# Performance work log

Hardware: AMD Instinct MI355X
Metric: run time of the kernel (lower is better)

Reference implementation:

```python
import jax, jax.numpy as jnp
import numpy as np

B, S, D_MODEL, H, D_KV = 2, 2048, 1024, 16, 64
NUM_BUCKETS, MAX_DIST = 32, 128


def _relative_position_bucket(rel_pos, num_buckets=NUM_BUCKETS, max_distance=MAX_DIST):
    # bidirectional (encoder) bucketing, matching T5Attention._relative_position_bucket
    nb = num_buckets // 2
    buckets = (rel_pos > 0).astype(jnp.int32) * nb
    rel = jnp.abs(rel_pos)
    max_exact = nb // 2
    is_small = rel < max_exact
    rel_f = jnp.maximum(rel.astype(jnp.float32), 1.0)  # guard log(0); masked by is_small anyway
    large = max_exact + (
        jnp.log(rel_f / max_exact) / np.log(max_distance / max_exact) * (nb - max_exact)
    ).astype(jnp.int32)
    large = jnp.minimum(large, nb - 1)
    return buckets + jnp.where(is_small, rel, large)


def setup_inputs() -> dict:
    key = jax.random.key(0)
    ks = jax.random.split(key, 6)
    sc = 1.0 / np.sqrt(D_MODEL)
    return {
        "hidden_states": jax.random.normal(ks[0], (B, S, D_MODEL), jnp.float32),
        "Wq": jax.random.normal(ks[1], (D_MODEL, H * D_KV), jnp.float32) * sc,
        "Wk": jax.random.normal(ks[2], (D_MODEL, H * D_KV), jnp.float32) * sc,
        "Wv": jax.random.normal(ks[3], (D_MODEL, H * D_KV), jnp.float32) * sc,
        "Wo": jax.random.normal(ks[4], (H * D_KV, D_MODEL), jnp.float32) * sc,
        "rel_bias_table": jax.random.normal(ks[5], (NUM_BUCKETS, H), jnp.float32),
    }


def reference(hidden_states, Wq, Wk, Wv, Wo, rel_bias_table):
    b, s, _ = hidden_states.shape
    # projections (T5 uses no bias, scale=1.0 in attention)
    q = (hidden_states @ Wq).reshape(b, s, H, D_KV).transpose(0, 2, 1, 3)  # bhsd
    k = (hidden_states @ Wk).reshape(b, s, H, D_KV).transpose(0, 2, 1, 3)
    v = (hidden_states @ Wv).reshape(b, s, H, D_KV).transpose(0, 2, 1, 3)

    # relative position bias: [1, H, S, S]
    ctx = jnp.arange(s)[:, None]
    mem = jnp.arange(s)[None, :]
    buckets = _relative_position_bucket(mem - ctx)          # [S, S]
    pos_bias = rel_bias_table[buckets]                       # [S, S, H]
    pos_bias = pos_bias.transpose(2, 0, 1)[None]             # [1, H, S, S]

    scores = jnp.einsum("bhqd,bhkd->bhqk", q, k) + pos_bias  # scale = 1.0
    probs = jax.nn.softmax(scores, axis=-1)
    attn = jnp.einsum("bhqk,bhkd->bhqd", probs, v)
    attn = attn.transpose(0, 2, 1, 3).reshape(b, s, H * D_KV)
    return attn @ Wo
```

## Files before the change

kernel.cpp:

```cpp
#include <hip/hip_runtime.h>
#include <hip/hip_fp16.h>

#define S_LEN 2048
#define NH 16
#define DK 64
#define DM 1024
#define NB 2
#define QKV_SZ (NB * NH * S_LEN * DK)

typedef _Float16 half8 __attribute__((ext_vector_type(8)));
typedef _Float16 half4v __attribute__((ext_vector_type(4)));
typedef __fp16 fp16x2 __attribute__((ext_vector_type(2)));
typedef float f32x4 __attribute__((ext_vector_type(4)));

static __device__ __forceinline__ half4v pack4(const f32x4 v) {
  fp16x2 lo = __builtin_amdgcn_cvt_pkrtz(v[0], v[1]);
  fp16x2 hi = __builtin_amdgcn_cvt_pkrtz(v[2], v[3]);
  half4v r;
  ((fp16x2*)&r)[0] = lo;
  ((fp16x2*)&r)[1] = hi;
  return r;
}

#define GLL(gp, lp)                                                              \
  __builtin_amdgcn_global_load_lds(                                              \
      (const __attribute__((address_space(1))) unsigned int*)(gp),               \
      (__attribute__((address_space(3))) unsigned int*)(lp), 16, 0, 0)

__global__ __launch_bounds__(256) void prep_kernel(
    const float* __restrict__ hs, const float* __restrict__ Wq,
    const float* __restrict__ Wk, const float* __restrict__ Wv,
    const float* __restrict__ Wo, _Float16* __restrict__ Xh,
    _Float16* __restrict__ Wqkvt, _Float16* __restrict__ Wot) {
  const int z = blockIdx.z;
  const int t = threadIdx.x;
  if (z < 4) {
    __shared__ float tile[32][33];
    const float* W = (z == 0) ? Wq : (z == 1) ? Wk : (z == 2) ? Wv : Wo;
    _Float16* Wt = (z < 3) ? (Wqkvt + (size_t)z * 1048576) : Wot;
    float scale = (z == 0) ? 1.44269504f : 1.0f;
    int tx = t & 31, ty = t >> 5;
    int nx = blockIdx.x * 32 + tx;
    int ky = blockIdx.y * 32;
#pragma unroll
    for (int i = 0; i < 32; i += 8) tile[ty + i][tx] = W[(size_t)(ky + ty + i) * DM + nx];
    __syncthreads();
    int kx = ky + tx;
    int ny = blockIdx.x * 32;
#pragma unroll
    for (int i = 0; i < 32; i += 8)
      Wt[(size_t)(ny + ty + i) * DM + kx] = (_Float16)(tile[tx][ty + i] * scale);
  } else {
    const int blk = blockIdx.x + (blockIdx.y << 5);
    const int n4 = (NB * S_LEN * DM) / 4;
    for (int i = blk * 256 + t; i < n4; i += 1024 * 256) {
      float4 v = ((const float4*)hs)[i];
      half4v o;
      o[0] = (_Float16)v.x; o[1] = (_Float16)v.y; o[2] = (_Float16)v.z; o[3] = (_Float16)v.w;
      ((half4v*)Xh)[i] = o;
    }
  }
}

template <int MODE>
__global__ __launch_bounds__(256) void gemm_f16(const _Float16* __restrict__ A,
                                                const _Float16* __restrict__ Bt,
                                                void* __restrict__ Cout,
                                                int M, int N, int K) {
  __shared__ _Float16 As[2][128 * 32];
  __shared__ _Float16 Bs[2][128 * 32];
  const int t = threadIdx.x;
  const int gx = gridDim.x;
  const int nwg = gx * gridDim.y;
  const int orig = blockIdx.x + gx * blockIdx.y;
  const int wg = (orig & 7) * (nwg >> 3) + (orig >> 3);
  const int m0 = (wg / gx) * 128, n0 = (wg % gx) * 128;
  const int w = t >> 6, lane = t & 63, l15 = lane & 15, quad = lane >> 4;
  const int wr = (w >> 1) * 64, wc = (w & 1) * 64;
  const int swz = (quad ^ (l15 & 3)) * 8;

  const int row0_ = t >> 2, cg0 = (t & 3) ^ (row0_ & 3);
  const int row1_ = (t + 256) >> 2, cg1 = ((t + 256) & 3) ^ (row1_ & 3);
  const int aof0 = row0_ * K + cg0 * 8, aof1 = row1_ * K + cg1 * 8;
  const int lda = t * 16, ldb = (t + 256) * 16;

  f32x4 acc[4][4];
#pragma unroll
  for (int i = 0; i < 4; i++)
#pragma unroll
    for (int j = 0; j < 4; j++) acc[i][j] = (f32x4){0.f, 0.f, 0.f, 0.f};

#define GSTAGE(bs, kk)                                                     \
  do {                                                                     \
    const _Float16* ap_ = A + (size_t)m0 * K + (kk);                       \
    const _Float16* bp_ = Bt + (size_t)n0 * K + (kk);                      \
    GLL(ap_ + aof0, (char*)As[bs] + lda);                                  \
    GLL(ap_ + aof1, (char*)As[bs] + ldb);                                  \
    GLL(bp_ + aof0, (char*)Bs[bs] + lda);                                  \
    GLL(bp_ + aof1, (char*)Bs[bs] + ldb);                                  \
  } while (0)

  GSTAGE(0, 0);
  __syncthreads();

#define GTILE(c, kk)                                                          \
  do {                                                                        \
    if ((kk) + 32 < K) GSTAGE((c) ^ 1, (kk) + 32);                            \
    half8 af[4], bf[4];                                                       \
    _Pragma("unroll") for (int i = 0; i < 4; i++)                             \
        af[i] = *(const half8*)(As[c] + (wr + i * 16 + l15) * 32 + swz);      \
    _Pragma("unroll") for (int i = 0; i < 4; i++)                             \
        bf[i] = *(const half8*)(Bs[c] + (wc + i * 16 + l15) * 32 + swz);      \
    _Pragma("unroll") for (int i = 0; i < 4; i++)                             \
        _Pragma("unroll") for (int j = 0; j < 4; j++)                         \
            acc[i][j] =                                                       \
                __builtin_amdgcn_mfma_f32_16x16x32_f16(af[i], bf[j], acc[i][j], 0, 0, 0); \
    __syncthreads();                                                          \
  } while (0)

  for (int k0 = 0; k0 < K; k0 += 64) {
    GTILE(0, k0);
    GTILE(1, k0 + 32);
  }
#undef GTILE
#undef GSTAGE

#pragma unroll
  for (int i = 0; i < 4; i++)
#pragma unroll
    for (int j = 0; j < 4; j++) {
      int row0 = m0 + wr + i * 16 + quad * 4;
      int col = n0 + wc + j * 16 + l15;
      if (MODE == 1) {
#pragma unroll
        for (int r = 0; r < 4; r++)
          ((float*)Cout)[(size_t)(row0 + r) * N + col] = acc[i][j][r];
      } else {
        int which = col >> 10, rem = col & 1023, hh = rem >> 6, dd = rem & 63;
        int bb = row0 >> 11, ss = row0 & 2047;
        _Float16* base = (_Float16*)Cout;
        if (which == 2) {
          *(half4v*)(base + (size_t)2 * QKV_SZ +
                     ((size_t)((bb * NH + hh) * DK + dd)) * S_LEN + ss) = pack4(acc[i][j]);
        } else {
#pragma unroll
          for (int r = 0; r < 4; r++)
            base[(size_t)which * QKV_SZ +
                 ((size_t)((bb * NH + hh) * S_LEN) + ss + r) * DK + dd] = (_Float16)acc[i][j][r];
        }
      }
    }
}

__global__ __launch_bounds__(256) void gemm_f16_n64(const _Float16* __restrict__ A,
                                                    const _Float16* __restrict__ Bt,
                                                    float* __restrict__ C,
                                                    int M, int N, int K) {
  __shared__ _Float16 As[2][128 * 32];
  __shared__ _Float16 Bs[2][64 * 32];
  const int t = threadIdx.x;
  const int gx = gridDim.x;
  const int nwg = gx * gridDim.y;
  const int orig = blockIdx.x + gx * blockIdx.y;
  const int wg = (orig & 7) * (nwg >> 3) + (orig >> 3);
  const int m0 = (wg / gx) * 128, n0 = (wg % gx) * 64;
  const int w = t >> 6, lane = t & 63, l15 = lane & 15, quad = lane >> 4;
  const int wr = (w >> 1) * 64, wc = (w & 1) * 32;
  const int swz = (quad ^ (l15 & 3)) * 8;

  const int row0_ = t >> 2, cg0 = (t & 3) ^ (row0_ & 3);
  const int row1_ = (t + 256) >> 2, cg1 = ((t + 256) & 3) ^ (row1_ & 3);
  const int aof0 = row0_ * K + cg0 * 8, aof1 = row1_ * K + cg1 * 8;
  const int lda = t * 16, ldb = (t + 256) * 16;

  f32x4 acc[4][2];
#pragma unroll
  for (int i = 0; i < 4; i++)
#pragma unroll
    for (int j = 0; j < 2; j++) acc[i][j] = (f32x4){0.f, 0.f, 0.f, 0.f};

#define GSTAGE(bs, kk)                                                     \
  do {                                                                     \
    const _Float16* ap_ = A + (size_t)m0 * K + (kk);                       \
    const _Float16* bp_ = Bt + (size_t)n0 * K + (kk);                      \
    GLL(ap_ + aof0, (char*)As[bs] + lda);                                  \
    GLL(ap_ + aof1, (char*)As[bs] + ldb);                                  \
    GLL(bp_ + aof0, (char*)Bs[bs] + lda);                                  \
  } while (0)

  GSTAGE(0, 0);
  __syncthreads();

#define GTILE(c, kk)                                                          \
  do {                                                                        \
    if ((kk) + 32 < K) GSTAGE((c) ^ 1, (kk) + 32);                            \
    half8 af[4], bf[2];                                                       \
    _Pragma("unroll") for (int i = 0; i < 4; i++)                             \
        af[i] = *(const half8*)(As[c] + (wr + i * 16 + l15) * 32 + swz);      \
    _Pragma("unroll") for (int j = 0; j < 2; j++)                             \
        bf[j] = *(const half8*)(Bs[c] + (wc + j * 16 + l15) * 32 + swz);      \
    _Pragma("unroll") for (int i = 0; i < 4; i++)                             \
        _Pragma("unroll") for (int j = 0; j < 2; j++)                         \
            acc[i][j] =                                                       \
                __builtin_amdgcn_mfma_f32_16x16x32_f16(af[i], bf[j], acc[i][j], 0, 0, 0); \
    __syncthreads();                                                          \
  } while (0)

  for (int k0 = 0; k0 < K; k0 += 64) {
    GTILE(0, k0);
    GTILE(1, k0 + 32);
  }
#undef GTILE
#undef GSTAGE

#pragma unroll
  for (int i = 0; i < 4; i++)
#pragma unroll
    for (int j = 0; j < 2; j++) {
      int row0 = m0 + wr + i * 16 + quad * 4;
      int col = n0 + wc + j * 16 + l15;
#pragma unroll
      for (int r = 0; r < 4; r++)
        C[(size_t)(row0 + r) * N + col] = acc[i][j][r];
    }
}

__global__ __launch_bounds__(256, 4) void attn_kernel(
    const _Float16* __restrict__ Q, const _Float16* __restrict__ K,
    const _Float16* __restrict__ Vt, const float* __restrict__ tbl,
    _Float16* __restrict__ attn_out) {
  __shared__ _Float16 Ks[2][4096];
  __shared__ _Float16 Vs[2][4096];
  __shared__ float slab[512];

  const int t = threadIdx.x;
  const int orig = blockIdx.x + (blockIdx.y << 5) + (blockIdx.z << 9);
  const int wg = (orig & 7) * 128 + (orig >> 3);
  const int Q0 = (wg & 31) * 64;
  const int h = (wg >> 5) & 15, b = wg >> 9;
  const int w = t >> 6, lane = t & 63, l15 = lane & 15, quad = lane >> 4;
  const int qw0 = Q0 + w * 16;
  const int sw7 = l15 & 7;

  const _Float16* Qb = Q + (size_t)(b * NH + h) * S_LEN * DK;
  const _Float16* Kb = K + (size_t)(b * NH + h) * S_LEN * DK;
  const _Float16* Vb = Vt + (size_t)(b * NH + h) * S_LEN * DK;

  for (int i = t; i < 512; i += 256) {
    int rel = i - 256;
    int bucket = rel > 0 ? 16 : 0;
    int a = rel < 0 ? -rel : rel;
    if (a < 8) {
      bucket += a;
    } else {
      int lg = 31 - __clz(a * a);
      int large = 8 + (lg - 6);
      bucket += (large < 15 ? large : 15);
    }
    slab[i] = tbl[bucket * NH + h] * 1.44269504f;
  }
  const float cbn = tbl[15 * NH + h] * 1.44269504f;
  const float cbp = tbl[31 * NH + h] * 1.44269504f;

  const int id0 = t, id1 = t + 256;
  const int r0_ = id0 >> 3, cg0 = (id0 & 7) ^ (r0_ & 7), p0 = r0_ & 31;
  const int sr0 = (r0_ & 32) | (((p0 >> 2) & 3) << 3) | ((p0 >> 4) << 2) | (p0 & 3);
  const int r1_ = id1 >> 3, cg1 = (id1 & 7) ^ (r1_ & 7), p1 = r1_ & 31;
  const int sr1 = (r1_ & 32) | (((p1 >> 2) & 3) << 3) | ((p1 >> 4) << 2) | (p1 & 3);
  const int kofa = sr0 * DK + cg0 * 8, kofb = sr1 * DK + cg1 * 8;
  const int vofa = r0_ * S_LEN + cg0 * 8, vofb = r1_ * S_LEN + cg1 * 8;
  const int lda = id0 * 16, ldb = id1 * 16;

#define STAGE(bs, kk0)                                   \
  do {                                                   \
    const _Float16* kp_ = Kb + (size_t)(kk0) * DK;       \
    const _Float16* vp_ = Vb + (kk0);                    \
    GLL(kp_ + kofa, (char*)Ks[bs] + lda);                \
    GLL(kp_ + kofb, (char*)Ks[bs] + ldb);                \
    GLL(vp_ + vofa, (char*)Vs[bs] + lda);                \
    GLL(vp_ + vofb, (char*)Vs[bs] + ldb);                \
  } while (0)

  half8 qf[2];
#pragma unroll
  for (int dh = 0; dh < 2; dh++)
    qf[dh] = *(const half8*)(Qb + (size_t)(qw0 + l15) * DK + dh * 32 + quad * 8);

  f32x4 o[4];
#pragma unroll
  for (int dt = 0; dt < 4; dt++) o[dt] = (f32x4){0.f, 0.f, 0.f, 0.f};
  f32x4 lac = (f32x4){0.f, 0.f, 0.f, 0.f};
  float m_ = -INFINITY;
  const half8 ones8 = {(_Float16)1.f, (_Float16)1.f, (_Float16)1.f, (_Float16)1.f,
                       (_Float16)1.f, (_Float16)1.f, (_Float16)1.f, (_Float16)1.f};

  const int rd0 = l15 * 64 + (quad ^ sw7) * 8;
  const int rd1 = rd0 ^ 32;

  STAGE(0, 0);
  __syncthreads();

#define TILE(c, kk, stage_ok)                                                         \
  do {                                                                                \
    if (stage_ok) STAGE((c) ^ 1, (kk) + 64);   \
    const int dk0 = (kk) - qw0;                                                       \
    const bool farneg = (dk0 <= -191);                                                \
    const bool farpos = (dk0 >= 143);                                                 \
    const bool nearc = !(farneg || farpos);                                           \
    const float cb = farneg ? cbn : cbp;                                              \
    f32x4 st[4];                                                                      \
    if (nearc) {                                                                      \
      _Pragma("unroll") for (int kt = 0; kt < 4; kt++) {                              \
        int i0 = dk0 + (kt >> 1) * 32 + quad * 8 + (kt & 1) * 4 - l15 + 256;          \
        f32x4 v_;                                                                     \
        v_[0] = slab[i0]; v_[1] = slab[i0 + 1];                                       \
        v_[2] = slab[i0 + 2]; v_[3] = slab[i0 + 3];                                   \
        st[kt] = v_;                                                                  \
      }                                                                               \
    } else {                                                                          \
      _Pragma("unroll") for (int kt = 0; kt < 4; kt++)                                \
          st[kt] = (f32x4){0.f, 0.f, 0.f, 0.f};                                       \
    }                                                                                 \
    half8 kf0[4], kf1[4];                                                             \
    _Pragma("unroll") for (int kt = 0; kt < 4; kt++) {                                \
      kf0[kt] = *(const half8*)(&Ks[c][rd0 + kt * 1024]);                             \
      kf1[kt] = *(const half8*)(&Ks[c][rd1 + kt * 1024]);                             \
    }                                                                                 \
    __builtin_amdgcn_s_setprio(1);                                                    \
    _Pragma("unroll") for (int kt = 0; kt < 4; kt++) {                                \
      st[kt] = __builtin_amdgcn_mfma_f32_16x16x32_f16(kf0[kt], qf[0], st[kt], 0, 0, 0); \
      st[kt] = __builtin_amdgcn_mfma_f32_16x16x32_f16(kf1[kt], qf[1], st[kt], 0, 0, 0); \
    }                                                                                 \
    __builtin_amdgcn_s_setprio(0);                                                    \
     \
      \
    half8 vfr[4][2];                                                                  \
    _Pragma("unroll") for (int dt = 0; dt < 4; dt++) {                                \
      vfr[dt][0] = *(const half8*)(&Vs[c][rd0 + dt * 1024]);                          \
      vfr[dt][1] = *(const half8*)(&Vs[c][rd1 + dt * 1024]);                          \
    }                                                                                 \
                                                         \
    float x0 = fmaxf(fmaxf(st[0][0], st[0][1]), st[0][2]);                            \
    float x1 = fmaxf(fmaxf(st[0][3], st[1][0]), st[1][1]);                            \
    float x2 = fmaxf(fmaxf(st[1][2], st[1][3]), st[2][0]);                            \
    float x3 = fmaxf(fmaxf(st[2][1], st[2][2]), st[2][3]);                            \
    float x4 = fmaxf(fmaxf(st[3][0], st[3][1]), st[3][2]);                            \
    float cm = fmaxf(fmaxf(fmaxf(x0, x1), fmaxf(x2, x3)), fmaxf(x4, st[3][3]));       \
    cm = fmaxf(cm, __shfl_xor(cm, 16));                                               \
    cm = fmaxf(cm, __shfl_xor(cm, 32));                                               \
    float mc = nearc ? cm : cm + cb;                                                  \
    if (__any(mc > m_ + 8.f)) {     \
      float mnew = fmaxf(m_, mc);                                                     \
      float alpha = __builtin_amdgcn_exp2f(m_ - mnew);                                \
      m_ = mnew;                                                                      \
      lac *= alpha;                                                                   \
      _Pragma("unroll") for (int dt = 0; dt < 4; dt++) o[dt] *= alpha;                \
    }                                                                                 \
    float msub = nearc ? m_ : m_ - cb;                                                \
    half8 pb0, pb1;                                                                   \
    _Pragma("unroll") for (int kt = 0; kt < 4; kt++) {                                \
      f32x4 p_;                                                                       \
      _Pragma("unroll") for (int r = 0; r < 4; r++)                                   \
          p_[r] = __builtin_amdgcn_exp2f(st[kt][r] - msub);                           \
      ((half4v*)((kt < 2) ? &pb0 : &pb1))[kt & 1] = pack4(p_);                        \
    }                                                                                 \
    __builtin_amdgcn_s_setprio(1);                                                    \
    \
    lac = __builtin_amdgcn_mfma_f32_16x16x32_f16(ones8, pb0, lac, 0, 0, 0);           \
    lac = __builtin_amdgcn_mfma_f32_16x16x32_f16(ones8, pb1, lac, 0, 0, 0);           \
                 \
    _Pragma("unroll") for (int dt = 0; dt < 4; dt++) {                                \
      o[dt] = __builtin_amdgcn_mfma_f32_16x16x32_f16(vfr[dt][0], pb0, o[dt], 0, 0, 0);\
      o[dt] = __builtin_amdgcn_mfma_f32_16x16x32_f16(vfr[dt][1], pb1, o[dt], 0, 0, 0);\
    }                                                                                 \
    __builtin_amdgcn_s_setprio(0);                                                    \
    __syncthreads();              \
  } while (0)

  for (int k0 = 0; k0 < S_LEN; k0 += 128) {
    TILE(0, k0, 1);
    TILE(1, k0 + 64, (k0 + 128 < S_LEN));
  }
#undef TILE
#undef STAGE

  float inv = 1.0f / lac[0];
  int q = qw0 + l15;
#pragma unroll
  for (int dt = 0; dt < 4; dt++) {
    f32x4 ov = o[dt] * inv;
    *(half4v*)(attn_out + ((size_t)(b * S_LEN + q)) * DM + h * DK + dt * 16 + quad * 4) =
        pack4(ov);
  }
}

extern "C" void kernel_launch(void* const* d_in, const int* in_sizes, int n_in,
                              void* d_out, int out_size, void* d_ws, size_t ws_size,
                              hipStream_t stream) {
  const float* hs  = (const float*)d_in[0];
  const float* Wq  = (const float*)d_in[1];
  const float* Wk  = (const float*)d_in[2];
  const float* Wv  = (const float*)d_in[3];
  const float* Wo  = (const float*)d_in[4];
  const float* tbl = (const float*)d_in[5];
  float* out = (float*)d_out;
  char* ws = (char*)d_ws;

  _Float16* Xh    = (_Float16*)(ws);
  _Float16* Wqkvt = (_Float16*)(ws + (8u << 20));
  _Float16* Wot   = (_Float16*)(ws + (14u << 20));
  _Float16* Qd    = (_Float16*)(ws + (16u << 20));
  _Float16* Kd    = Qd + (size_t)QKV_SZ;
  _Float16* Vd    = Qd + (size_t)2 * QKV_SZ;
  _Float16* Ah    = (_Float16*)(ws + (40u << 20));

  prep_kernel<<<dim3(32, 32, 5), 256, 0, stream>>>(hs, Wq, Wk, Wv, Wo, Xh, Wqkvt, Wot);
  gemm_f16<0><<<dim3(24, 32), 256, 0, stream>>>(Xh, Wqkvt, (void*)Qd, NB * S_LEN, 3 * DM, DM);
  attn_kernel<<<dim3(S_LEN / 64, NH, NB), 256, 0, stream>>>(Qd, Kd, Vd, tbl, Ah);
  gemm_f16_n64<<<dim3(16, 32), 256, 0, stream>>>(Ah, Wot, out, NB * S_LEN, DM, DM);
}
```

Baseline: 194.0 us.

## Process two 16-row query subtiles per wave to double K/V fragment reuse

Each wave now handles 32 query rows as two 16-row subtiles instead of one, so every workgroup covers 128 queries and the grid is halved. Each K and V fragment read from LDS feeds twice as many MFMAs, which halves total K/V global staging and LDS read traffic per query. In exchange, register pressure roughly doubles: launch bounds drop from 4 to 2 blocks per CU, and there are only 512 workgroups, which cuts occupancy and the latency hiding it provides.

```diff
diff --git a/kernel.cpp b/kernel.cpp
--- a/kernel.cpp
+++ b/kernel.cpp
@@ -225,7 +225,7 @@
     }
 }
 
-__global__ __launch_bounds__(256, 4) void attn_kernel(
+__global__ __launch_bounds__(256, 2) void attn_kernel(
     const _Float16* __restrict__ Q, const _Float16* __restrict__ K,
     const _Float16* __restrict__ Vt, const float* __restrict__ tbl,
     _Float16* __restrict__ attn_out) {
@@ -234,12 +234,12 @@
   __shared__ float slab[512];
 
   const int t = threadIdx.x;
-  const int orig = blockIdx.x + (blockIdx.y << 5) + (blockIdx.z << 9);
-  const int wg = (orig & 7) * 128 + (orig >> 3);
-  const int Q0 = (wg & 31) * 64;
-  const int h = (wg >> 5) & 15, b = wg >> 9;
+  const int orig = blockIdx.x + (blockIdx.y << 4) + (blockIdx.z << 8);
+  const int wg = (orig & 7) * 64 + (orig >> 3);
+  const int Q0 = (wg & 15) * 128;
+  const int h = (wg >> 4) & 15, b = wg >> 8;
   const int w = t >> 6, lane = t & 63, l15 = lane & 15, quad = lane >> 4;
-  const int qw0 = Q0 + w * 16;
+  const int qw0 = Q0 + w * 32;
   const int sw7 = l15 & 7;
 
   const _Float16* Qb = Q + (size_t)(b * NH + h) * S_LEN * DK;
@@ -281,16 +281,20 @@
     GLL(vp_ + vofb, (char*)Vs[bs] + ldb);                \
   } while (0)
 
-  half8 qf[2];
-#pragma unroll
-  for (int dh = 0; dh < 2; dh++)
-    qf[dh] = *(const half8*)(Qb + (size_t)(qw0 + l15) * DK + dh * 32 + quad * 8);
-
-  f32x4 o[4];
-#pragma unroll
-  for (int dt = 0; dt < 4; dt++) o[dt] = (f32x4){0.f, 0.f, 0.f, 0.f};
-  f32x4 lac = (f32x4){0.f, 0.f, 0.f, 0.f};
-  float m_ = -INFINITY;
+  half8 qf[2][2];
+#pragma unroll
+  for (int u = 0; u < 2; u++)
+#pragma unroll
+    for (int dh = 0; dh < 2; dh++)
+      qf[dh][u] = *(const half8*)(Qb + (size_t)(qw0 + u * 16 + l15) * DK + dh * 32 + quad * 8);
+
+  f32x4 o[4][2];
+#pragma unroll
+  for (int dt = 0; dt < 4; dt++)
+#pragma unroll
+    for (int u = 0; u < 2; u++) o[dt][u] = (f32x4){0.f, 0.f, 0.f, 0.f};
+  f32x4 lac[2] = {(f32x4){0.f, 0.f, 0.f, 0.f}, (f32x4){0.f, 0.f, 0.f, 0.f}};
+  float m_[2] = {-INFINITY, -INFINITY};
   const half8 ones8 = {(_Float16)1.f, (_Float16)1.f, (_Float16)1.f, (_Float16)1.f,
                        (_Float16)1.f, (_Float16)1.f, (_Float16)1.f, (_Float16)1.f};
 
@@ -303,23 +307,27 @@
 #define TILE(c, kk, stage_ok)                                                         \
   do {                                                                                \
     if (stage_ok) STAGE((c) ^ 1, (kk) + 64);   \
-    const int dk0 = (kk) - qw0;                                                       \
-    const bool farneg = (dk0 <= -191);                                                \
-    const bool farpos = (dk0 >= 143);                                                 \
-    const bool nearc = !(farneg || farpos);                                           \
-    const float cb = farneg ? cbn : cbp;                                              \
-    f32x4 st[4];                                                                      \
-    if (nearc) {                                                                      \
-      _Pragma("unroll") for (int kt = 0; kt < 4; kt++) {                              \
-        int i0 = dk0 + (kt >> 1) * 32 + quad * 8 + (kt & 1) * 4 - l15 + 256;          \
-        f32x4 v_;                                                                     \
-        v_[0] = slab[i0]; v_[1] = slab[i0 + 1];                                       \
-        v_[2] = slab[i0 + 2]; v_[3] = slab[i0 + 3];                                   \
-        st[kt] = v_;                                                                  \
+    f32x4 st[2][4];                                                                   \
+    bool nearc[2];                                                                    \
+    float cb[2];                                                                      \
+    _Pragma("unroll") for (int u = 0; u < 2; u++) {                                   \
+      const int dk0 = (kk) - qw0 - u * 16;                                            \
+      const bool farneg = (dk0 <= -191);                                              \
+      const bool farpos = (dk0 >= 143);                                               \
+      nearc[u] = !(farneg || farpos);                                                 \
+      cb[u] = farneg ? cbn : cbp;                                                     \
+      if (nearc[u]) {                                                                 \
+        _Pragma("unroll") for (int kt = 0; kt < 4; kt++) {                            \
+          int i0 = dk0 + (kt >> 1) * 32 + quad * 8 + (kt & 1) * 4 - l15 + 256;        \
+          f32x4 v_;                                                                   \
+          v_[0] = slab[i0]; v_[1] = slab[i0 + 1];                                     \
+          v_[2] = slab[i0 + 2]; v_[3] = slab[i0 + 3];                                 \
+          st[u][kt] = v_;                                                             \
+        }                                                                             \
+      } else {                                                                        \
+        _Pragma("unroll") for (int kt = 0; kt < 4; kt++)                              \
+            st[u][kt] = (f32x4){0.f, 0.f, 0.f, 0.f};                                  \
       }                                                                               \
-    } else {                                                                          \
-      _Pragma("unroll") for (int kt = 0; kt < 4; kt++)                                \
-          st[kt] = (f32x4){0.f, 0.f, 0.f, 0.f};                                       \
     }                                                                                 \
     half8 kf0[4], kf1[4];                                                             \
     _Pragma("unroll") for (int kt = 0; kt < 4; kt++) {                                \
@@ -327,52 +335,54 @@
       kf1[kt] = *(const half8*)(&Ks[c][rd1 + kt * 1024]);                             \
     }                                                                                 \
     __builtin_amdgcn_s_setprio(1);                                                    \
-    _Pragma("unroll") for (int kt = 0; kt < 4; kt++) {                                \
-      st[kt] = __builtin_amdgcn_mfma_f32_16x16x32_f16(kf0[kt], qf[0], st[kt], 0, 0, 0); \
-      st[kt] = __builtin_amdgcn_mfma_f32_16x16x32_f16(kf1[kt], qf[1], st[kt], 0, 0, 0); \
-    }                                                                                 \
+    _Pragma("unroll") for (int kt = 0; kt < 4; kt++)                                  \
+      _Pragma("unroll") for (int u = 0; u < 2; u++) {                                 \
+        st[u][kt] = __builtin_amdgcn_mfma_f32_16x16x32_f16(kf0[kt], qf[0][u], st[u][kt], 0, 0, 0); \
+        st[u][kt] = __builtin_amdgcn_mfma_f32_16x16x32_f16(kf1[kt], qf[1][u], st[u][kt], 0, 0, 0); \
+      }                                                                               \
     __builtin_amdgcn_s_setprio(0);                                                    \
-     \
-      \
+       \
     half8 vfr[4][2];                                                                  \
     _Pragma("unroll") for (int dt = 0; dt < 4; dt++) {                                \
       vfr[dt][0] = *(const half8*)(&Vs[c][rd0 + dt * 1024]);                          \
       vfr[dt][1] = *(const half8*)(&Vs[c][rd1 + dt * 1024]);                          \
     }                                                                                 \
-                                                         \
-    float x0 = fmaxf(fmaxf(st[0][0], st[0][1]), st[0][2]);                            \
-    float x1 = fmaxf(fmaxf(st[0][3], st[1][0]), st[1][1]);                            \
-    float x2 = fmaxf(fmaxf(st[1][2], st[1][3]), st[2][0]);                            \
-    float x3 = fmaxf(fmaxf(st[2][1], st[2][2]), st[2][3]);                            \
-    float x4 = fmaxf(fmaxf(st[3][0], st[3][1]), st[3][2]);                            \
-    float cm = fmaxf(fmaxf(fmaxf(x0, x1), fmaxf(x2, x3)), fmaxf(x4, st[3][3]));       \
-    cm = fmaxf(cm, __shfl_xor(cm, 16));                                               \
-    cm = fmaxf(cm, __shfl_xor(cm, 32));                                               \
-    float mc = nearc ? cm : cm + cb;                                                  \
-    if (__any(mc > m_ + 8.f)) {     \
-      float mnew = fmaxf(m_, mc);                                                     \
-      float alpha = __builtin_amdgcn_exp2f(m_ - mnew);                                \
-      m_ = mnew;                                                                      \
-      lac *= alpha;                                                                   \
-      _Pragma("unroll") for (int dt = 0; dt < 4; dt++) o[dt] *= alpha;                \
-    }                                                                                 \
-    float msub = nearc ? m_ : m_ - cb;                                                \
-    half8 pb0, pb1;                                                                   \
-    _Pragma("unroll") for (int kt = 0; kt < 4; kt++) {                                \
-      f32x4 p_;                                                                       \
-      _Pragma("unroll") for (int r = 0; r < 4; r++)                                   \
-          p_[r] = __builtin_amdgcn_exp2f(st[kt][r] - msub);                           \
-      ((half4v*)((kt < 2) ? &pb0 : &pb1))[kt & 1] = pack4(p_);                        \
+    half8 pb0[2], pb1[2];                                                             \
+    _Pragma("unroll") for (int u = 0; u < 2; u++) {                                   \
+      float x0 = fmaxf(fmaxf(st[u][0][0], st[u][0][1]), st[u][0][2]);                 \
+      float x1 = fmaxf(fmaxf(st[u][0][3], st[u][1][0]), st[u][1][1]);                 \
+      float x2 = fmaxf(fmaxf(st[u][1][2], st[u][1][3]), st[u][2][0]);                 \
+      float x3 = fmaxf(fmaxf(st[u][2][1], st[u][2][2]), st[u][2][3]);                 \
+      float x4 = fmaxf(fmaxf(st[u][3][0], st[u][3][1]), st[u][3][2]);                 \
+      float cm = fmaxf(fmaxf(fmaxf(x0, x1), fmaxf(x2, x3)), fmaxf(x4, st[u][3][3]));  \
+      cm = fmaxf(cm, __shfl_xor(cm, 16));                                             \
+      cm = fmaxf(cm, __shfl_xor(cm, 32));                                             \
+      float mc = nearc[u] ? cm : cm + cb[u];                                          \
+      if (__any(mc > m_[u] + 8.f)) {                               \
+        float mnew = fmaxf(m_[u], mc);                                                \
+        float alpha = __builtin_amdgcn_exp2f(m_[u] - mnew);                           \
+        m_[u] = mnew;                                                                 \
+        lac[u] *= alpha;                                                              \
+        _Pragma("unroll") for (int dt = 0; dt < 4; dt++) o[dt][u] *= alpha;           \
+      }                                                                               \
+      float msub = nearc[u] ? m_[u] : m_[u] - cb[u];                                  \
+      _Pragma("unroll") for (int kt = 0; kt < 4; kt++) {                              \
+        f32x4 p_;                                                                     \
+        _Pragma("unroll") for (int r = 0; r < 4; r++)                                 \
+            p_[r] = __builtin_amdgcn_exp2f(st[u][kt][r] - msub);                      \
+        ((half4v*)((kt < 2) ? &pb0[u] : &pb1[u]))[kt & 1] = pack4(p_);                \
+      }                                                                               \
     }                                                                                 \
     __builtin_amdgcn_s_setprio(1);                                                    \
-    \
-    lac = __builtin_amdgcn_mfma_f32_16x16x32_f16(ones8, pb0, lac, 0, 0, 0);           \
-    lac = __builtin_amdgcn_mfma_f32_16x16x32_f16(ones8, pb1, lac, 0, 0, 0);           \
-                 \
-    _Pragma("unroll") for (int dt = 0; dt < 4; dt++) {                                \
-      o[dt] = __builtin_amdgcn_mfma_f32_16x16x32_f16(vfr[dt][0], pb0, o[dt], 0, 0, 0);\
-      o[dt] = __builtin_amdgcn_mfma_f32_16x16x32_f16(vfr[dt][1], pb1, o[dt], 0, 0, 0);\
+    _Pragma("unroll") for (int u = 0; u < 2; u++) {                                   \
+      lac[u] = __builtin_amdgcn_mfma_f32_16x16x32_f16(ones8, pb0[u], lac[u], 0, 0, 0);\
+      lac[u] = __builtin_amdgcn_mfma_f32_16x16x32_f16(ones8, pb1[u], lac[u], 0, 0, 0);\
     }                                                                                 \
+    _Pragma("unroll") for (int dt = 0; dt < 4; dt++)                                  \
+      _Pragma("unroll") for (int u = 0; u < 2; u++) {                                 \
+        o[dt][u] = __builtin_amdgcn_mfma_f32_16x16x32_f16(vfr[dt][0], pb0[u], o[dt][u], 0, 0, 0); \
+        o[dt][u] = __builtin_amdgcn_mfma_f32_16x16x32_f16(vfr[dt][1], pb1[u], o[dt][u], 0, 0, 0); \
+      }                                                                               \
     __builtin_amdgcn_s_setprio(0);                                                    \
     __syncthreads();              \
   } while (0)
@@ -384,13 +394,16 @@
 #undef TILE
 #undef STAGE
 
-  float inv = 1.0f / lac[0];
-  int q = qw0 + l15;
-#pragma unroll
-  for (int dt = 0; dt < 4; dt++) {
-    f32x4 ov = o[dt] * inv;
-    *(half4v*)(attn_out + ((size_t)(b * S_LEN + q)) * DM + h * DK + dt * 16 + quad * 4) =
-        pack4(ov);
+#pragma unroll
+  for (int u = 0; u < 2; u++) {
+    float inv = 1.0f / lac[u][0];
+    int q = qw0 + u * 16 + l15;
+#pragma unroll
+    for (int dt = 0; dt < 4; dt++) {
+      f32x4 ov = o[dt][u] * inv;
+      *(half4v*)(attn_out + ((size_t)(b * S_LEN + q)) * DM + h * DK + dt * 16 + quad * 4) =
+          pack4(ov);
+    }
   }
 }
 
@@ -416,6 +429,6 @@
 
   prep_kernel<<<dim3(32, 32, 5), 256, 0, stream>>>(hs, Wq, Wk, Wv, Wo, Xh, Wqkvt, Wot);
   gemm_f16<0><<<dim3(24, 32), 256, 0, stream>>>(Xh, Wqkvt, (void*)Qd, NB * S_LEN, 3 * DM, DM);
-  attn_kernel<<<dim3(S_LEN / 64, NH, NB), 256, 0, stream>>>(Qd, Kd, Vd, tbl, Ah);
+  attn_kernel<<<dim3(S_LEN / 128, NH, NB), 256, 0, stream>>>(Qd, Kd, Vd, tbl, Ah);
   gemm_f16_n64<<<dim3(16, 32), 256, 0, stream>>>(Ah, Wot, out, NB * S_LEN, DM, DM);
 }
```

Result: no change. 193.6 us (-0.2%).
